# Kernel optimization log

Measured on AMD Instinct MI355X. Metric: run time of the kernel, lower is better.

Reference implementation:

```python
import jax, jax.numpy as jnp
import numpy as np

SIZE = 33
PAD = SIZE // 2
NUM_CLASSES = 19
LOG19 = float(np.log(19.0))
EPS = 1e-6


def _box_sum(x):
    """Depthwise 33x33 all-ones box-sum with zero padding, done separably.
    x: [N, C, H, W] -> [N, C, H, W]
    """
    c = x.shape[1]
    kh = jnp.ones((c, 1, SIZE, 1), x.dtype)
    kw = jnp.ones((c, 1, 1, SIZE), x.dtype)
    dn = ('NCHW', 'OIHW', 'NCHW')
    y = jax.lax.conv_general_dilated(x, kh, (1, 1), [(PAD, PAD), (0, 0)],
                                     dimension_numbers=dn, feature_group_count=c)
    y = jax.lax.conv_general_dilated(y, kw, (1, 1), [(0, 0), (PAD, PAD)],
                                     dimension_numbers=dn, feature_group_count=c)
    return y


def setup_inputs() -> dict:
    key = jax.random.key(0)
    logit = jax.random.normal(key, (1, NUM_CLASSES, 1024, 2048), dtype=jnp.float32)
    return {"logit": logit}


def reference(logit):
    x = logit[0]                                   # [C, H, W]
    p = jax.nn.softmax(x, axis=0)                  # [C, H, W]
    # normalized per-pixel entropy, [1, 1, H, W]
    pixel_entropy = (jnp.sum(-p * jnp.log(p + EPS), axis=0) / LOG19)[None, None]
    region_sum_entropy = _box_sum(pixel_entropy)   # [1, 1, H, W]

    predict = jnp.argmax(p, axis=0)                # [H, W] int
    one_hot = jax.nn.one_hot(predict, NUM_CLASSES, dtype=jnp.float32)  # [H, W, C]
    one_hot = jnp.transpose(one_hot, (2, 0, 1))[None]                  # [1, C, H, W]
    summary = _box_sum(one_hot)                    # per-class region counts
    count = jnp.sum(summary, axis=1, keepdims=True)  # [1, 1, H, W] (= window size)
    dist = summary / count
    region_impurity = jnp.sum(-dist * jnp.log(dist + EPS), axis=1, keepdims=True) / LOG19
    prediction_uncertainty = region_sum_entropy / count
    score = region_impurity * prediction_uncertainty
    return score[0, 0], region_impurity[0, 0], prediction_uncertainty[0, 0]
```

## Files before the change

### kernel.cpp

```cpp
#include <hip/hip_runtime.h>
#include <hip/hip_fp16.h>

#define H 1024
#define W 2048
#define HW (H * W)
#define LOG19 2.9444389791664403f
#define TY 8
#define NT 576
#define NVERT 528
#define BCOLS 1024
#define PCOLS 1056
#define NG 132
#define GRP 41
#define LGS 9
#define GSS 11

typedef __attribute__((ext_vector_type(4))) float f32x4;
typedef __attribute__((ext_vector_type(2))) unsigned int u32x2;
typedef __attribute__((ext_vector_type(4))) unsigned int u32x4;

static __device__ __forceinline__ unsigned short f2h_bits(float f) {
    __half h = __float2half_rn(f);
    unsigned short b;
    __builtin_memcpy(&b, &h, 2);
    return b;
}
static __device__ __forceinline__ float h2f_bits(unsigned int b) {
    unsigned short s = (unsigned short)b;
    __half h;
    __builtin_memcpy(&h, &s, 2);
    return __half2float(h);
}

__global__ __launch_bounds__(256) void k1_entropy_argmax(
    const float* __restrict__ logit,
    unsigned int* __restrict__ packed) {
    int q = blockIdx.x * 256 + threadIdx.x;
    int p0 = q * 4;
    f32x4 v[19];
#pragma unroll
    for (int c = 0; c < 19; c++)
        v[c] = *reinterpret_cast<const f32x4*>(logit + (size_t)c * HW + p0);
    f32x4 m = v[0];
    int am[4] = {0, 0, 0, 0};
#pragma unroll
    for (int c = 1; c < 19; c++) {
#pragma unroll
        for (int j = 0; j < 4; j++)
            if (v[c][j] > m[j]) { m[j] = v[c][j]; am[j] = c; }
    }
    f32x4 S = (f32x4)(0.f), T = (f32x4)(0.f);
#pragma unroll
    for (int c = 0; c < 19; c++) {
#pragma unroll
        for (int j = 0; j < 4; j++) {
            float d = v[c][j] - m[j];
            float e = __expf(d);
            S[j] += e;
            T[j] += d * e;
        }
    }
    u32x4 w;
#pragma unroll
    for (int j = 0; j < 4; j++) {
        float ent = (__logf(S[j]) - T[j] / S[j]) * (1.0f / LOG19);
        w[j] = (unsigned int)f2h_bits(ent) | ((unsigned int)am[j] << 24);
    }
    *reinterpret_cast<u32x4*>(packed + p0) = w;
}

#define VACC(yy, SGN)                                                                   \
    if (vvalid) {                                                                       \
        u32x2 pw = *reinterpret_cast<const u32x2*>(packed + (size_t)(yy)*W + gcol0);    \
        _Pragma("unroll") for (int j = 0; j < 2; j++) {                                 \
            unsigned int wv = pw[j];                                                    \
            unsigned int cc = wv >> 24;                                                 \
            unsigned int wi = cc >> 2, bit = 1u << ((cc & 3u) * 8u);                    \
            _Pragma("unroll") for (int k = 0; k < 5; k++)                               \
                vc[j * 5 + k] SGN## = (wi == (unsigned)k) ? bit : 0u;                   \
            ve[j] SGN## = h2f_bits(wv);                                                 \
        }                                                                               \
    }
#define VSLIDE(y)                         \
    {                                     \
        int ya = (y) + 17, yr = (y) - 16; \
        if (ya < H) VACC(ya, +)           \
        if (yr >= 0) VACC(yr, -)          \
    }
#define PUBLISH(b)                                                              \
    if (tid < NVERT) {                                                          \
        unsigned int ps[10];                                                    \
        float pe = ve[0] + ve[1];                                               \
        _Pragma("unroll") for (int k = 0; k < 5; k++) {                         \
            ps[2 * k] = (vc[k] & 0x00FF00FFu) + (vc[5 + k] & 0x00FF00FFu);      \
            ps[2 * k + 1] = ((vc[k] >> 8) & 0x00FF00FFu) +                      \
                            ((vc[5 + k] >> 8) & 0x00FF00FFu);                   \
        }                                                                       \
        int g = tid >> 2, sl0 = (2 * tid) & 7;                                  \
        _Pragma("unroll") for (int k = 0; k < 5; k++) {                         \
            lcnt[b][g * GRP + sl0 * 5 + k] = vc[k];                             \
            lcnt[b][g * GRP + (sl0 + 1) * 5 + k] = vc[5 + k];                   \
        }                                                                       \
        lent[b][g * LGS + sl0] = ve[0];                                         \
        lent[b][g * LGS + sl0 + 1] = ve[1];                                     \
        _Pragma("unroll") for (int q = 0; q < 10; q++) {                        \
            ps[q] += __shfl_xor(ps[q], 1);                                      \
            ps[q] += __shfl_xor(ps[q], 2);                                      \
        }                                                                       \
        pe += __shfl_xor(pe, 1);                                                \
        pe += __shfl_xor(pe, 2);                                                \
        if ((tid & 3) == 0) {                                                   \
            _Pragma("unroll") for (int q = 0; q < 10; q++)                      \
                gsum[b][g * GSS + q] = ps[q];                                   \
            gsum[b][g * GSS + 10] = __float_as_uint(pe);                        \
        }                                                                       \
    }

__global__ __launch_bounds__(NT) void k23_box_score(
    const unsigned int* __restrict__ packed,
    float* __restrict__ out_score,
    float* __restrict__ out_imp,
    float* __restrict__ out_unc) {
    __shared__ float lut[1090];
    __shared__ unsigned int lcnt[2][NG * GRP];
    __shared__ float lent[2][NG * LGS];
    __shared__ unsigned int gsum[2][NG * GSS];
    int tid = threadIdx.x;
    int bid = blockIdx.x;
    int xcd = bid & 7, idx = bid >> 3;
    int strip = xcd * 16 + (idx >> 1);
    int colbase = (idx & 1) * BCOLS;
    int y0 = strip * TY;

    for (int n = tid; n < 1090; n += NT)
        lut[n] = n ? (float)n * __logf((float)n) : 0.f;

    int gcol0 = colbase - 16 + 2 * tid;
    bool vvalid = (tid < NVERT) && ((unsigned)gcol0 < (unsigned)W);
    unsigned int vc[10];
#pragma unroll
    for (int i = 0; i < 10; i++) vc[i] = 0u;
    float ve[2] = {0.f, 0.f};
    {
        int ylo = max(y0 - 16, 0), yhi = min(y0 + 16, H - 1);
        for (int yy = ylo; yy <= yhi; yy++) VACC(yy, +)
    }

#pragma unroll
    for (int p = 0; p < TY / 2; p++) {
        int yA = y0 + 2 * p;
        PUBLISH(0)
        VSLIDE(yA)
        PUBLISH(1)
        __syncthreads();

        if (tid < 256) {
            int rsel = tid >> 7;
            int hq = tid & 127;
            int x0h = hq * 8;
            int y = yA + rsel;
            unsigned int ha[10];
            float hes;
            {
#pragma unroll
                for (int q = 0; q < 10; q++)
                    ha[q] = gsum[rsel][hq * GSS + q] + gsum[rsel][(hq + 1) * GSS + q] +
                            gsum[rsel][(hq + 2) * GSS + q] + gsum[rsel][(hq + 3) * GSS + q];
                hes = __uint_as_float(gsum[rsel][hq * GSS + 10]) +
                      __uint_as_float(gsum[rsel][(hq + 1) * GSS + 10]) +
                      __uint_as_float(gsum[rsel][(hq + 2) * GSS + 10]) +
                      __uint_as_float(gsum[rsel][(hq + 3) * GSS + 10]);
#pragma unroll
                for (int k = 0; k < 5; k++) {
                    unsigned int wv = lcnt[rsel][(hq + 4) * GRP + k];
                    ha[2 * k] += wv & 0x00FF00FFu;
                    ha[2 * k + 1] += (wv >> 8) & 0x00FF00FFu;
                }
                hes += lent[rsel][(hq + 4) * LGS];
            }
            int rcount = min(y + 16, H - 1) - max(y - 16, 0) + 1;
            f32x4 osc[2], oim[2], oun[2];
#pragma unroll
            for (int s = 0; s < 8; s++) {
                int gx = colbase + x0h + s;
                int ccount = min(gx + 16, W - 1) - max(gx - 16, 0) + 1;
                int Tw = rcount * ccount;
                float invT = 1.0f / (float)Tw;
                float sum = 0.f;
#pragma unroll
                for (int k = 0; k < 5; k++) {
                    unsigned int a = ha[2 * k], b = ha[2 * k + 1];
                    sum += lut[a & 0xFFFFu] + lut[b & 0xFFFFu] + lut[a >> 16];
                    if (k < 4) sum += lut[b >> 16];
                }
                float imp = (lut[Tw] - sum) * invT * (1.0f / LOG19);
                float unc = hes * invT;
                osc[s >> 2][s & 3] = imp * unc;
                oim[s >> 2][s & 3] = imp;
                oun[s >> 2][s & 3] = unc;
                if (s < 7) {
                    int ga = hq + ((s + 33) >> 3), ja = (s + 33) & 7;
                    hes += lent[rsel][ga * LGS + ja] - lent[rsel][hq * LGS + s];
#pragma unroll
                    for (int k = 0; k < 5; k++) {
                        unsigned int wa = lcnt[rsel][ga * GRP + ja * 5 + k];
                        unsigned int wr = lcnt[rsel][hq * GRP + s * 5 + k];
                        ha[2 * k] += (wa & 0x00FF00FFu) - (wr & 0x00FF00FFu);
                        ha[2 * k + 1] += ((wa >> 8) & 0x00FF00FFu) - ((wr >> 8) & 0x00FF00FFu);
                    }
                }
            }
            size_t qo = (size_t)y * W + colbase + x0h;
            *reinterpret_cast<f32x4*>(out_score + qo) = osc[0];
            *reinterpret_cast<f32x4*>(out_score + qo + 4) = osc[1];
            *reinterpret_cast<f32x4*>(out_imp + qo) = oim[0];
            *reinterpret_cast<f32x4*>(out_imp + qo + 4) = oim[1];
            *reinterpret_cast<f32x4*>(out_unc + qo) = oun[0];
            *reinterpret_cast<f32x4*>(out_unc + qo + 4) = oun[1];
        }
        if (p < TY / 2 - 1) VSLIDE(yA + 1)
        __syncthreads();
    }
}

extern "C" void kernel_launch(void* const* d_in, const int* in_sizes, int n_in,
                              void* d_out, int out_size, void* d_ws, size_t ws_size,
                              hipStream_t stream) {
    const float* logit = (const float*)d_in[0];
    float* out = (float*)d_out;
    unsigned int* packed = (unsigned int*)d_ws;

    k1_entropy_argmax<<<HW / 1024, 256, 0, stream>>>(logit, packed);
    k23_box_score<<<256, NT, 0, stream>>>(packed, out, out + HW, out + 2 * HW);
}
```

Before: 72.53 us.

## Fuse entropy/argmax and box-score kernels into one cooperative grid-synced kernel

Merges the per-pixel softmax entropy/argmax pass into the box-score kernel. Each block first computes the packed entropy/class words for its own 8-row strip while 64 threads build the log LUT, then a cooperative grid sync is taken before the sliding-window phase. The change also uses nontemporal loads for the logits and nontemporal stores for the outputs, and moves the second vertical slide ahead of the horizontal compute. Only 256 blocks do the first phase, so it may get less memory-level parallelism than the separate 2048-block kernel, and the grid sync adds its own cost.

Measured after the change: 112.3 us. 54.8% more time.

```diff
diff --git a/kernel.cpp b/kernel.cpp
--- a/kernel.cpp
+++ b/kernel.cpp
@@ -1,5 +1,7 @@
 #include <hip/hip_runtime.h>
 #include <hip/hip_fp16.h>
+#include <hip/hip_cooperative_groups.h>
+namespace cg = cooperative_groups;
 
 #define H 1024
 #define W 2048
@@ -9,21 +11,20 @@
 #define NT 576
 #define NVERT 528
 #define BCOLS 1024
-#define PCOLS 1056
 #define NG 132
 #define GRP 41
 #define LGS 9
 #define GSS 11
 
 typedef __attribute__((ext_vector_type(4))) float f32x4;
+typedef __attribute__((ext_vector_type(2))) float f32x2;
 typedef __attribute__((ext_vector_type(2))) unsigned int u32x2;
-typedef __attribute__((ext_vector_type(4))) unsigned int u32x4;
-
-static __device__ __forceinline__ unsigned short f2h_bits(float f) {
+
+static __device__ __forceinline__ unsigned int f2h_bits(float f) {
     __half h = __float2half_rn(f);
     unsigned short b;
     __builtin_memcpy(&b, &h, 2);
-    return b;
+    return (unsigned int)b;
 }
 static __device__ __forceinline__ float h2f_bits(unsigned int b) {
     unsigned short s = (unsigned short)b;
@@ -32,54 +33,17 @@
     return __half2float(h);
 }
 
-__global__ __launch_bounds__(256) void k1_entropy_argmax(
-    const float* __restrict__ logit,
-    unsigned int* __restrict__ packed) {
-    int q = blockIdx.x * 256 + threadIdx.x;
-    int p0 = q * 4;
-    f32x4 v[19];
-#pragma unroll
-    for (int c = 0; c < 19; c++)
-        v[c] = *reinterpret_cast<const f32x4*>(logit + (size_t)c * HW + p0);
-    f32x4 m = v[0];
-    int am[4] = {0, 0, 0, 0};
-#pragma unroll
-    for (int c = 1; c < 19; c++) {
-#pragma unroll
-        for (int j = 0; j < 4; j++)
-            if (v[c][j] > m[j]) { m[j] = v[c][j]; am[j] = c; }
-    }
-    f32x4 S = (f32x4)(0.f), T = (f32x4)(0.f);
-#pragma unroll
-    for (int c = 0; c < 19; c++) {
-#pragma unroll
-        for (int j = 0; j < 4; j++) {
-            float d = v[c][j] - m[j];
-            float e = __expf(d);
-            S[j] += e;
-            T[j] += d * e;
-        }
-    }
-    u32x4 w;
-#pragma unroll
-    for (int j = 0; j < 4; j++) {
-        float ent = (__logf(S[j]) - T[j] / S[j]) * (1.0f / LOG19);
-        w[j] = (unsigned int)f2h_bits(ent) | ((unsigned int)am[j] << 24);
-    }
-    *reinterpret_cast<u32x4*>(packed + p0) = w;
-}
-
-#define VACC(yy, SGN)                                                                   \
-    if (vvalid) {                                                                       \
-        u32x2 pw = *reinterpret_cast<const u32x2*>(packed + (size_t)(yy)*W + gcol0);    \
-        _Pragma("unroll") for (int j = 0; j < 2; j++) {                                 \
-            unsigned int wv = pw[j];                                                    \
-            unsigned int cc = wv >> 24;                                                 \
-            unsigned int wi = cc >> 2, bit = 1u << ((cc & 3u) * 8u);                    \
-            _Pragma("unroll") for (int k = 0; k < 5; k++)                               \
-                vc[j * 5 + k] SGN## = (wi == (unsigned)k) ? bit : 0u;                   \
-            ve[j] SGN## = h2f_bits(wv);                                                 \
-        }                                                                               \
+#define VACC(yy, SGN)                                                                 \
+    if (vvalid) {                                                                     \
+        u32x2 pw = *reinterpret_cast<const u32x2*>(packed + (size_t)(yy)*W + gcol0);  \
+        _Pragma("unroll") for (int j = 0; j < 2; j++) {                               \
+            unsigned int wv = pw[j];                                                  \
+            unsigned int cc = wv >> 24;                                               \
+            unsigned int wi = cc >> 2, bit = 1u << ((cc & 3u) * 8u);                  \
+            _Pragma("unroll") for (int k = 0; k < 5; k++)                             \
+                vc[j * 5 + k] SGN## = (wi == (unsigned)k) ? bit : 0u;                 \
+            ve[j] SGN## = h2f_bits(wv);                                               \
+        }                                                                             \
     }
 #define VSLIDE(y)                         \
     {                                     \
@@ -116,8 +80,9 @@
         }                                                                       \
     }
 
-__global__ __launch_bounds__(NT) void k23_box_score(
-    const unsigned int* __restrict__ packed,
+__global__ __launch_bounds__(NT, 3) void fused_frs(
+    const float* __restrict__ logit,
+    unsigned int* __restrict__ packed,
     float* __restrict__ out_score,
     float* __restrict__ out_imp,
     float* __restrict__ out_unc) {
@@ -132,8 +97,47 @@
     int colbase = (idx & 1) * BCOLS;
     int y0 = strip * TY;
 
-    for (int n = tid; n < 1090; n += NT)
-        lut[n] = n ? (float)n * __logf((float)n) : 0.f;
+    if (tid >= 512) {
+        for (int n = tid - 512; n < 1090; n += 64)
+            lut[n] = n ? (float)n * __logf((float)n) : 0.f;
+    } else {
+        for (int it = 0; it < 8; ++it) {
+            int pp = (it << 9) | tid;
+            int row = y0 + (pp >> 9);
+            int col = colbase + ((pp & 511) << 1);
+            size_t p0 = (size_t)row * W + col;
+            f32x2 v[19];
+#pragma unroll
+            for (int c = 0; c < 19; c++)
+                v[c] = __builtin_nontemporal_load(
+                    reinterpret_cast<const f32x2*>(logit + (size_t)c * HW + p0));
+            f32x2 m = v[0];
+            int am0 = 0, am1 = 0;
+#pragma unroll
+            for (int c = 1; c < 19; c++) {
+                if (v[c][0] > m[0]) { m[0] = v[c][0]; am0 = c; }
+                if (v[c][1] > m[1]) { m[1] = v[c][1]; am1 = c; }
+            }
+            f32x2 S = {0.f, 0.f}, T = {0.f, 0.f};
+#pragma unroll
+            for (int c = 0; c < 19; c++) {
+#pragma unroll
+                for (int j = 0; j < 2; j++) {
+                    float d = v[c][j] - m[j];
+                    float e = __expf(d);
+                    S[j] += e;
+                    T[j] += d * e;
+                }
+            }
+            u32x2 wout;
+            wout[0] = f2h_bits((__logf(S[0]) - T[0] / S[0]) * (1.f / LOG19)) |
+                      ((unsigned)am0 << 24);
+            wout[1] = f2h_bits((__logf(S[1]) - T[1] / S[1]) * (1.f / LOG19)) |
+                      ((unsigned)am1 << 24);
+            *reinterpret_cast<u32x2*>(packed + p0) = wout;
+        }
+    }
+    cg::this_grid().sync();
 
     int gcol0 = colbase - 16 + 2 * tid;
     bool vvalid = (tid < NVERT) && ((unsigned)gcol0 < (unsigned)W);
@@ -153,6 +157,8 @@
         VSLIDE(yA)
         PUBLISH(1)
         __syncthreads();
+
+        if (p < TY / 2 - 1) VSLIDE(yA + 1)
 
         if (tid < 256) {
             int rsel = tid >> 7;
@@ -211,14 +217,13 @@
                 }
             }
             size_t qo = (size_t)y * W + colbase + x0h;
-            *reinterpret_cast<f32x4*>(out_score + qo) = osc[0];
-            *reinterpret_cast<f32x4*>(out_score + qo + 4) = osc[1];
-            *reinterpret_cast<f32x4*>(out_imp + qo) = oim[0];
-            *reinterpret_cast<f32x4*>(out_imp + qo + 4) = oim[1];
-            *reinterpret_cast<f32x4*>(out_unc + qo) = oun[0];
-            *reinterpret_cast<f32x4*>(out_unc + qo + 4) = oun[1];
+            __builtin_nontemporal_store(osc[0], reinterpret_cast<f32x4*>(out_score + qo));
+            __builtin_nontemporal_store(osc[1], reinterpret_cast<f32x4*>(out_score + qo + 4));
+            __builtin_nontemporal_store(oim[0], reinterpret_cast<f32x4*>(out_imp + qo));
+            __builtin_nontemporal_store(oim[1], reinterpret_cast<f32x4*>(out_imp + qo + 4));
+            __builtin_nontemporal_store(oun[0], reinterpret_cast<f32x4*>(out_unc + qo));
+            __builtin_nontemporal_store(oun[1], reinterpret_cast<f32x4*>(out_unc + qo + 4));
         }
-        if (p < TY / 2 - 1) VSLIDE(yA + 1)
         __syncthreads();
     }
 }
@@ -229,7 +234,11 @@
     const float* logit = (const float*)d_in[0];
     float* out = (float*)d_out;
     unsigned int* packed = (unsigned int*)d_ws;
-
-    k1_entropy_argmax<<<HW / 1024, 256, 0, stream>>>(logit, packed);
-    k23_box_score<<<256, NT, 0, stream>>>(packed, out, out + HW, out + 2 * HW);
-}
+    float* o_score = out;
+    float* o_imp = out + HW;
+    float* o_unc = out + 2 * HW;
+
+    void* args[] = {(void*)&logit, (void*)&packed, (void*)&o_score, (void*)&o_imp,
+                    (void*)&o_unc};
+    hipLaunchCooperativeKernel((void*)fused_frs, dim3(256), dim3(NT), args, 0, stream);
+}
```
